# Kernel optimization log

Hardware: AMD Instinct MI355X
Metric: run time of the kernel (lower is better)

## Reference

```python
import jax, jax.numpy as jnp
import numpy as np

N, D, NUM_CLASSES = 4096, 512, 128
MARGIN = 0.3


def setup_inputs() -> dict:
    key = jax.random.key(0)
    k1, k2 = jax.random.split(key)
    embeddings = jax.random.normal(k1, (N, D), dtype=jnp.float32)
    labels = jax.random.randint(k2, (N,), 0, NUM_CLASSES, dtype=jnp.int64)
    return {"embeddings": embeddings, "labels": labels}


def _batch_hard_triplet(embeddings, labels, margin):
    # L2-normalize rows (torch F.normalize: x / max(||x||, eps))
    norm = jnp.linalg.norm(embeddings, axis=1, keepdims=True)
    e = embeddings / jnp.maximum(norm, 1e-12)
    n = e.shape[0]
    # Pairwise Euclidean distance via Gram matrix; ||a-b||^2 = 2 - 2 a.b for unit vectors
    gram = e @ e.T                                   # [N, N]
    sq = jnp.clip(2.0 - 2.0 * gram, 0.0, None)
    # safe sqrt: zero (and exactly-equal) pairs get distance 0 with zero gradient
    nz = sq > 0
    dist = jnp.where(nz, jnp.sqrt(jnp.where(nz, sq, 1.0)), 0.0)  # [N, N]

    same = labels[:, None] == labels[None, :]        # [N, N] bool
    eye = jnp.eye(n, dtype=bool)
    pos_mask = same & ~eye                           # positives excluding self
    neg_mask = ~same

    # hardest positive (row max over positives), hardest negative (row min over negatives)
    dist_ap = jnp.max(jnp.where(pos_mask, dist, -jnp.inf), axis=1)  # [N]
    dist_an = jnp.min(jnp.where(neg_mask, dist, jnp.inf), axis=1)   # [N]

    valid = jnp.any(pos_mask, axis=1) & jnp.any(neg_mask, axis=1)   # rows kept by torch loop
    per_row = jax.nn.relu(dist_ap - dist_an + margin)
    num_valid = jnp.sum(valid)
    loss_sum = jnp.sum(jnp.where(valid, per_row, 0.0))
    return jnp.where(num_valid > 0, loss_sum / jnp.maximum(num_valid, 1), 0.0)


def reference(embeddings, labels):
    return _batch_hard_triplet(embeddings, labels, MARGIN)
```

## Files before the change

### kernel.cpp

```cpp
#include <hip/hip_runtime.h>
#include <hip/hip_bf16.h>
#include <stdint.h>


#define NROW 4096
#define DIM  512
#define MARGIN 0.3f
#define BT 128
#define KITERS 16
#define NTILE (NROW / BT)
#define NPAIR (NTILE * (NTILE + 1) / 2)
#define POS_INIT 0xFFFFFFFFu
#define NEG_INIT 0u

typedef __attribute__((ext_vector_type(8))) __bf16 bf16x8;
typedef __attribute__((ext_vector_type(4))) float  f32x4;

__device__ __forceinline__ unsigned enc(float f) {
    unsigned u = __float_as_uint(f);
    return (u & 0x80000000u) ? ~u : (u | 0x80000000u);
}
__device__ __forceinline__ float dec(unsigned e) {
    return (e & 0x80000000u) ? __uint_as_float(e & 0x7fffffffu)
                             : __uint_as_float(~e);
}
__device__ __forceinline__ unsigned short f2bf(float f) {
    __hip_bfloat16 h = __float2bfloat16(f);
    return *reinterpret_cast<unsigned short*>(&h);
}

__global__ void tl_norm(const float* __restrict__ E,
                        char* __restrict__ Epack,
                        unsigned* __restrict__ posArr,
                        unsigned* __restrict__ negArr) {
    if (blockIdx.x < 16) {
        int t = blockIdx.x * 256 + threadIdx.x;
        posArr[t] = POS_INIT;
        negArr[t] = NEG_INIT;
    }
    const int wave = threadIdx.x >> 6;
    const int lane = threadIdx.x & 63;
    const int row  = blockIdx.x * 4 + wave;

    const float4* src = (const float4*)(E + (size_t)row * DIM);
    float4 v0 = src[lane];
    float4 v1 = src[lane + 64];
    float ss = v0.x*v0.x + v0.y*v0.y + v0.z*v0.z + v0.w*v0.w
             + v1.x*v1.x + v1.y*v1.y + v1.z*v1.z + v1.w*v1.w;
    #pragma unroll
    for (int m = 32; m >= 1; m >>= 1) ss += __shfl_xor(ss, m);
    float inv = 1.0f / fmaxf(sqrtf(ss), 1e-12f);

    ushort4 o0, o1;
    o0.x = f2bf(v0.x * inv); o0.y = f2bf(v0.y * inv);
    o0.z = f2bf(v0.z * inv); o0.w = f2bf(v0.w * inv);
    o1.x = f2bf(v1.x * inv); o1.y = f2bf(v1.y * inv);
    o1.z = f2bf(v1.z * inv); o1.w = f2bf(v1.w * inv);

    const int g  = row >> 4;
    const int r  = row & 15;
    const int kbA = lane >> 3;
    const int q   = (lane >> 1) & 3;
    const int sub = (lane & 1) * 8;
    const size_t laneOff = (size_t)(q * 16 + r) * 16 + sub;
    char* base = Epack + (size_t)(g * 16) * 1024;
    *(ushort4*)(base + (size_t)(kbA    ) * 1024 + laneOff) = o0;
    *(ushort4*)(base + (size_t)(kbA + 8) * 1024 + laneOff) = o1;
}

__global__ void __launch_bounds__(256, 2)
tl_gram(const char* __restrict__ Epack,
        const int* __restrict__ labels,
        unsigned* __restrict__ posArr,
        unsigned* __restrict__ negArr) {
    __shared__ int rowLab[BT];
    __shared__ int colLab[BT];

    int t = blockIdx.x, bi = 0, rowlen = NTILE;
    while (t >= rowlen) { t -= rowlen; rowlen--; bi++; }
    const int bj = bi + t;

    const int tid  = threadIdx.x;
    const int wave = tid >> 6;
    const int lane = tid & 63;
    const int quad = lane >> 4;
    const int l16  = lane & 15;
    const int wr   = wave >> 1;
    const int wc   = wave & 1;
    const int tileI = bi * BT;
    const int tileJ = bj * BT;
    const bool diag = (bi == bj);

    if (tid < BT) rowLab[tid] = labels[tileI + tid];
    else          colLab[tid - BT] = labels[tileJ + (tid - BT)];
    __syncthreads();

    const char* aP[4];
    const char* bP[4];
    #pragma unroll
    for (int mi = 0; mi < 4; mi++)
        aP[mi] = Epack + (size_t)(tileI / 16 + wr * 4 + mi) * 16384 + (size_t)lane * 16;
    #pragma unroll
    for (int ni = 0; ni < 4; ni++)
        bP[ni] = Epack + (size_t)(tileJ / 16 + wc * 4 + ni) * 16384 + (size_t)lane * 16;

    f32x4 acc[4][4] = {};

    #pragma unroll
    for (int kc = 0; kc < KITERS; kc++) {
        bf16x8 a[4], b[4];
        #pragma unroll
        for (int mi = 0; mi < 4; mi++)
            a[mi] = *(const bf16x8*)(aP[mi] + kc * 1024);
        #pragma unroll
        for (int ni = 0; ni < 4; ni++)
            b[ni] = *(const bf16x8*)(bP[ni] + kc * 1024);

        #pragma unroll
        for (int mi = 0; mi < 4; mi++)
            #pragma unroll
            for (int ni = 0; ni < 4; ni++)
                acc[mi][ni] = __builtin_amdgcn_mfma_f32_16x16x32_bf16(
                    a[mi], b[ni], acc[mi][ni], 0, 0, 0);
    }

    int rl[16], cl[4], clocv[4];
    #pragma unroll
    for (int mi = 0; mi < 4; mi++)
        #pragma unroll
        for (int reg = 0; reg < 4; reg++)
            rl[mi * 4 + reg] = rowLab[wr * 64 + mi * 16 + quad * 4 + reg];
    #pragma unroll
    for (int ni = 0; ni < 4; ni++) {
        clocv[ni] = wc * 64 + ni * 16 + l16;
        cl[ni] = colLab[clocv[ni]];
    }

    #pragma unroll
    for (int mi = 0; mi < 4; mi++) {
        #pragma unroll
        for (int reg = 0; reg < 4; reg++) {
            const int rloc = wr * 64 + mi * 16 + quad * 4 + reg;
            const int lr   = rl[mi * 4 + reg];
            const int gi   = tileI + rloc;
            float pmin =  INFINITY;
            float nmax = -INFINITY;
            #pragma unroll
            for (int ni = 0; ni < 4; ni++) {
                const int gj  = tileJ + clocv[ni];
                const float g = acc[mi][ni][reg];
                const bool same = (lr == cl[ni]);
                if (same && gi != gj) pmin = fminf(pmin, g);
                if (!same)            nmax = fmaxf(nmax, g);
            }
            #pragma unroll
            for (int m = 1; m < 16; m <<= 1) {
                pmin = fminf(pmin, __shfl_xor(pmin, m));
                nmax = fmaxf(nmax, __shfl_xor(nmax, m));
            }
            if (l16 == 0) {
                if (pmin <  INFINITY) atomicMin(&posArr[gi], enc(pmin));
                if (nmax > -INFINITY) atomicMax(&negArr[gi], enc(nmax));
            }
        }
    }

    if (!diag) {
        #pragma unroll
        for (int ni = 0; ni < 4; ni++) {
            const int lc = cl[ni];
            const int gj = tileJ + clocv[ni];
            float pmin =  INFINITY;
            float nmax = -INFINITY;
            #pragma unroll
            for (int mi = 0; mi < 4; mi++) {
                #pragma unroll
                for (int reg = 0; reg < 4; reg++) {
                    const float g = acc[mi][ni][reg];
                    const bool same = (rl[mi * 4 + reg] == lc);
                    if (same) pmin = fminf(pmin, g);
                    else      nmax = fmaxf(nmax, g);
                }
            }
            pmin = fminf(pmin, __shfl_xor(pmin, 16));
            pmin = fminf(pmin, __shfl_xor(pmin, 32));
            nmax = fmaxf(nmax, __shfl_xor(nmax, 16));
            nmax = fmaxf(nmax, __shfl_xor(nmax, 32));
            if (quad == 0) {
                if (pmin <  INFINITY) atomicMin(&posArr[gj], enc(pmin));
                if (nmax > -INFINITY) atomicMax(&negArr[gj], enc(nmax));
            }
        }
    }
}

__global__ void tl_final(const unsigned* __restrict__ posArr,
                         const unsigned* __restrict__ negArr,
                         float* __restrict__ out) {
    const int tid = threadIdx.x;
    float sum = 0.0f;
    int   count = 0;
    for (int i = tid; i < NROW; i += 256) {
        const unsigned pe = posArr[i];
        const unsigned ne = negArr[i];
        const bool valid = (pe != POS_INIT) && (ne != NEG_INIT);
        const float dap = sqrtf(fmaxf(2.0f - 2.0f * dec(pe), 0.0f));
        const float dan = sqrtf(fmaxf(2.0f - 2.0f * dec(ne), 0.0f));
        const float per = fmaxf(dap - dan + MARGIN, 0.0f);
        if (valid) { sum += per; count += 1; }
    }
    #pragma unroll
    for (int m = 32; m >= 1; m >>= 1) {
        sum   += __shfl_xor(sum, m);
        count += __shfl_xor(count, m);
    }
    __shared__ float ssum[4];
    __shared__ int   scnt[4];
    const int wave = tid >> 6, lane = tid & 63;
    if (lane == 0) { ssum[wave] = sum; scnt[wave] = count; }
    __syncthreads();
    if (tid == 0) {
        float s = ssum[0] + ssum[1] + ssum[2] + ssum[3];
        int   c = scnt[0] + scnt[1] + scnt[2] + scnt[3];
        out[0] = (c > 0) ? (s / (float)c) : 0.0f;
    }
}

extern "C" void kernel_launch(void* const* d_in, const int* in_sizes, int n_in,
                              void* d_out, int out_size, void* d_ws, size_t ws_size,
                              hipStream_t stream) {
    const float* E      = (const float*)d_in[0];
    const int*   labels = (const int*)d_in[1];
    float*       out    = (float*)d_out;

    char* ws = (char*)d_ws;
    char* Epack           = ws;
    unsigned* posArr      = (unsigned*)(ws + (size_t)NROW * DIM * 2);
    unsigned* negArr      = posArr + NROW;

    tl_norm<<<NROW / 4, 256, 0, stream>>>(E, Epack, posArr, negArr);
    tl_gram<<<NPAIR, 256, 0, stream>>>(Epack, labels, posArr, negArr);
    tl_final<<<1, 256, 0, stream>>>(posArr, negArr, out);
}
```

Before: 93.57 us.

## Fuse final reduction into gram kernel via last-block counter; coalesce norm writes

Removes the separate single-block final kernel by having the last gram block, detected with an atomic completion counter, perform the loss reduction. The norm kernel now handles 16 rows per block and stages the bf16 rows in LDS, so the packed-layout stores are written as contiguous 16-byte chunks instead of scattered 8-byte ones. This saves one launch and its gap, and improves write coalescing. In exchange it adds a threadfence and an atomic per gram block, plus a serial tail on the last block.

After: 119.7 us. 27.9% more time.

```diff
diff --git a/kernel.cpp b/kernel.cpp
--- a/kernel.cpp
+++ b/kernel.cpp
@@ -29,52 +29,73 @@
     return *reinterpret_cast<unsigned short*>(&h);
 }
 
+#define LROW 520
 __global__ void tl_norm(const float* __restrict__ E,
                         char* __restrict__ Epack,
                         unsigned* __restrict__ posArr,
-                        unsigned* __restrict__ negArr) {
+                        unsigned* __restrict__ negArr,
+                        unsigned* __restrict__ doneCnt) {
+    __shared__ __align__(16) unsigned short sm[16 * LROW];
+    const int tid  = threadIdx.x;
+    const int wave = tid >> 6;
+    const int lane = tid & 63;
+
     if (blockIdx.x < 16) {
-        int t = blockIdx.x * 256 + threadIdx.x;
+        int t = blockIdx.x * 256 + tid;
         posArr[t] = POS_INIT;
         negArr[t] = NEG_INIT;
-    }
-    const int wave = threadIdx.x >> 6;
-    const int lane = threadIdx.x & 63;
-    const int row  = blockIdx.x * 4 + wave;
-
-    const float4* src = (const float4*)(E + (size_t)row * DIM);
-    float4 v0 = src[lane];
-    float4 v1 = src[lane + 64];
-    float ss = v0.x*v0.x + v0.y*v0.y + v0.z*v0.z + v0.w*v0.w
-             + v1.x*v1.x + v1.y*v1.y + v1.z*v1.z + v1.w*v1.w;
-    #pragma unroll
-    for (int m = 32; m >= 1; m >>= 1) ss += __shfl_xor(ss, m);
-    float inv = 1.0f / fmaxf(sqrtf(ss), 1e-12f);
-
-    ushort4 o0, o1;
-    o0.x = f2bf(v0.x * inv); o0.y = f2bf(v0.y * inv);
-    o0.z = f2bf(v0.z * inv); o0.w = f2bf(v0.w * inv);
-    o1.x = f2bf(v1.x * inv); o1.y = f2bf(v1.y * inv);
-    o1.z = f2bf(v1.z * inv); o1.w = f2bf(v1.w * inv);
-
-    const int g  = row >> 4;
-    const int r  = row & 15;
-    const int kbA = lane >> 3;
-    const int q   = (lane >> 1) & 3;
-    const int sub = (lane & 1) * 8;
-    const size_t laneOff = (size_t)(q * 16 + r) * 16 + sub;
-    char* base = Epack + (size_t)(g * 16) * 1024;
-    *(ushort4*)(base + (size_t)(kbA    ) * 1024 + laneOff) = o0;
-    *(ushort4*)(base + (size_t)(kbA + 8) * 1024 + laneOff) = o1;
+        if (t == 0) *doneCnt = 0;
+    }
+
+    const int rowBase = blockIdx.x * 16;
+
+    #pragma unroll
+    for (int rr = 0; rr < 4; rr++) {
+        const int r   = wave * 4 + rr;
+        const int row = rowBase + r;
+        const float4* src = (const float4*)(E + (size_t)row * DIM);
+        float4 v0 = src[lane];
+        float4 v1 = src[lane + 64];
+        float ss = v0.x*v0.x + v0.y*v0.y + v0.z*v0.z + v0.w*v0.w
+                 + v1.x*v1.x + v1.y*v1.y + v1.z*v1.z + v1.w*v1.w;
+        #pragma unroll
+        for (int m = 32; m >= 1; m >>= 1) ss += __shfl_xor(ss, m);
+        float inv = 1.0f / fmaxf(sqrtf(ss), 1e-12f);
+
+        ushort4 o0, o1;
+        o0.x = f2bf(v0.x * inv); o0.y = f2bf(v0.y * inv);
+        o0.z = f2bf(v0.z * inv); o0.w = f2bf(v0.w * inv);
+        o1.x = f2bf(v1.x * inv); o1.y = f2bf(v1.y * inv);
+        o1.z = f2bf(v1.z * inv); o1.w = f2bf(v1.w * inv);
+        *(ushort4*)&sm[r * LROW + 4 * lane]       = o0;
+        *(ushort4*)&sm[r * LROW + 256 + 4 * lane] = o1;
+    }
+    __syncthreads();
+
+    char* outB = Epack + (size_t)blockIdx.x * 16384;
+    const int r = tid & 15;
+    const int q = (tid >> 4) & 3;
+    #pragma unroll
+    for (int p = 0; p < 4; p++) {
+        const int kb = p * 4 + wave;
+        const int ks = kb * 32 + q * 8;
+        ulonglong2 val = *(const ulonglong2*)&sm[r * LROW + ks];
+        *(ulonglong2*)(outB + (size_t)(p * 256 + tid) * 16) = val;
+    }
 }
 
 __global__ void __launch_bounds__(256, 2)
 tl_gram(const char* __restrict__ Epack,
         const int* __restrict__ labels,
         unsigned* __restrict__ posArr,
-        unsigned* __restrict__ negArr) {
+        unsigned* __restrict__ negArr,
+        unsigned* __restrict__ doneCnt,
+        float* __restrict__ out) {
     __shared__ int rowLab[BT];
     __shared__ int colLab[BT];
+    __shared__ int lastFlag;
+    __shared__ float ssum[4];
+    __shared__ int   scnt[4];
 
     int t = blockIdx.x, bi = 0, rowlen = NTILE;
     while (t >= rowlen) { t -= rowlen; rowlen--; bi++; }
@@ -192,37 +213,38 @@
             }
         }
     }
-}
-
-__global__ void tl_final(const unsigned* __restrict__ posArr,
-                         const unsigned* __restrict__ negArr,
-                         float* __restrict__ out) {
-    const int tid = threadIdx.x;
-    float sum = 0.0f;
-    int   count = 0;
-    for (int i = tid; i < NROW; i += 256) {
-        const unsigned pe = posArr[i];
-        const unsigned ne = negArr[i];
-        const bool valid = (pe != POS_INIT) && (ne != NEG_INIT);
-        const float dap = sqrtf(fmaxf(2.0f - 2.0f * dec(pe), 0.0f));
-        const float dan = sqrtf(fmaxf(2.0f - 2.0f * dec(ne), 0.0f));
-        const float per = fmaxf(dap - dan + MARGIN, 0.0f);
-        if (valid) { sum += per; count += 1; }
-    }
-    #pragma unroll
-    for (int m = 32; m >= 1; m >>= 1) {
-        sum   += __shfl_xor(sum, m);
-        count += __shfl_xor(count, m);
-    }
-    __shared__ float ssum[4];
-    __shared__ int   scnt[4];
-    const int wave = tid >> 6, lane = tid & 63;
-    if (lane == 0) { ssum[wave] = sum; scnt[wave] = count; }
+
+    __threadfence();
+    if (tid == 0) {
+        unsigned prev = atomicAdd(doneCnt, 1u);
+        lastFlag = (prev == NPAIR - 1) ? 1 : 0;
+    }
     __syncthreads();
-    if (tid == 0) {
-        float s = ssum[0] + ssum[1] + ssum[2] + ssum[3];
-        int   c = scnt[0] + scnt[1] + scnt[2] + scnt[3];
-        out[0] = (c > 0) ? (s / (float)c) : 0.0f;
+    if (lastFlag) {
+        __threadfence();
+        float sum = 0.0f;
+        int   count = 0;
+        for (int i = tid; i < NROW; i += 256) {
+            const unsigned pe = atomicOr(&posArr[i], 0u);
+            const unsigned ne = atomicOr(&negArr[i], 0u);
+            const bool valid = (pe != POS_INIT) && (ne != NEG_INIT);
+            const float dap = sqrtf(fmaxf(2.0f - 2.0f * dec(pe), 0.0f));
+            const float dan = sqrtf(fmaxf(2.0f - 2.0f * dec(ne), 0.0f));
+            const float per = fmaxf(dap - dan + MARGIN, 0.0f);
+            if (valid) { sum += per; count += 1; }
+        }
+        #pragma unroll
+        for (int m = 32; m >= 1; m >>= 1) {
+            sum   += __shfl_xor(sum, m);
+            count += __shfl_xor(count, m);
+        }
+        if (lane == 0) { ssum[wave] = sum; scnt[wave] = count; }
+        __syncthreads();
+        if (tid == 0) {
+            float s = ssum[0] + ssum[1] + ssum[2] + ssum[3];
+            int   c = scnt[0] + scnt[1] + scnt[2] + scnt[3];
+            out[0] = (c > 0) ? (s / (float)c) : 0.0f;
+        }
     }
 }
 
@@ -237,8 +259,8 @@
     char* Epack           = ws;
     unsigned* posArr      = (unsigned*)(ws + (size_t)NROW * DIM * 2);
     unsigned* negArr      = posArr + NROW;
-
-    tl_norm<<<NROW / 4, 256, 0, stream>>>(E, Epack, posArr, negArr);
-    tl_gram<<<NPAIR, 256, 0, stream>>>(Epack, labels, posArr, negArr);
-    tl_final<<<1, 256, 0, stream>>>(posArr, negArr, out);
-}
+    unsigned* doneCnt     = negArr + NROW;
+
+    tl_norm<<<NROW / 16, 256, 0, stream>>>(E, Epack, posArr, negArr, doneCnt);
+    tl_gram<<<NPAIR, 256, 0, stream>>>(Epack, labels, posArr, negArr, doneCnt, out);
+}
```
